# Kernel optimization log

Measured on AMD Instinct MI355X. Metric: run time of the kernel, lower is better.

The kernel has to match this reference:

```python
import jax, jax.numpy as jnp
import numpy as np
from jax import lax

VOCAB = 32000
EMBED = 1024
HIDDEN = 1024
ML = 64          # config.MAX_LENGTH
L = 50           # input sentence length
HH = HIDDEN // 2 # per-direction encoder hidden


def _lstm_cell(x, h, c, Wih, Whh, bih, bhh):
    # torch LSTM gate order: i, f, g, o
    g = x @ Wih.T + h @ Whh.T + bih + bhh
    i, f, gg, o = jnp.split(g, 4)
    i = jax.nn.sigmoid(i)
    f = jax.nn.sigmoid(f)
    gg = jnp.tanh(gg)
    o = jax.nn.sigmoid(o)
    c = f * c + i * gg
    return o * jnp.tanh(c), c


def setup_inputs() -> dict:
    key = jax.random.key(0)
    ks = jax.random.split(key, 24)
    def n(k, shape, s=0.05):
        return jax.random.normal(k, shape, jnp.float32) * s
    return {
        "x_tokens": jax.random.randint(ks[0], (L,), 0, VOCAB, jnp.int32),
        "allowed_mask": jnp.ones((VOCAB + ML,), jnp.float32),
        "embedding": n(ks[1], (VOCAB, EMBED)),
        # encoder bi-LSTM (two cells, each hidden//2)
        "Wih_f": n(ks[2], (4 * HH, EMBED)), "Whh_f": n(ks[3], (4 * HH, HH)),
        "bih_f": n(ks[4], (4 * HH,)), "bhh_f": n(ks[5], (4 * HH,)),
        "Wih_b": n(ks[6], (4 * HH, EMBED)), "Whh_b": n(ks[7], (4 * HH, HH)),
        "bih_b": n(ks[8], (4 * HH,)), "bhh_b": n(ks[9], (4 * HH,)),
        # decoder LSTM: input = embed + 2*hidden
        "Wih_d": n(ks[10], (4 * HIDDEN, EMBED + 2 * HIDDEN)),
        "Whh_d": n(ks[11], (4 * HIDDEN, HIDDEN)),
        "bih_d": n(ks[12], (4 * HIDDEN,)), "bhh_d": n(ks[13], (4 * HIDDEN,)),
        # attention: Linear(2*hidden -> MAX_LENGTH)
        "attn_W": n(ks[14], (ML, 2 * HIDDEN)), "attn_b": n(ks[15], (ML,)),
        # generate layer: Linear(hidden -> vocab)
        "gen_W": n(ks[16], (VOCAB, HIDDEN)), "gen_b": n(ks[17], (VOCAB,)),
        # copy layer: Linear(hidden -> hidden)
        "copy_W": n(ks[18], (HIDDEN, HIDDEN)), "copy_b": n(ks[19], (HIDDEN,)),
    }


def _forward(allowed_mask, embedding, Wih_f, Whh_f, bih_f, bhh_f,
             Wih_b, Whh_b, bih_b, bhh_b, Wih_d, Whh_d, bih_d, bhh_d,
             attn_W, attn_b, gen_W, gen_b, copy_W, copy_b, x_tokens):
    xemb = embedding[x_tokens]  # (L, EMBED)

    # --- encoder: two LSTM cells both stepped forward-in-time (as in the
    # original, where the bidirectional LSTM is called one token at a time) ---
    def enc_step(carry, xe):
        hf, cf, hb, cb = carry
        hf, cf = _lstm_cell(xe, hf, cf, Wih_f, Whh_f, bih_f, bhh_f)
        hb, cb = _lstm_cell(xe, hb, cb, Wih_b, Whh_b, bih_b, bhh_b)
        return (hf, cf, hb, cb), jnp.concatenate([hf, hb])

    z = jnp.zeros((HH,), xemb.dtype)
    (hf, cf, hb, cb), enc = lax.scan(enc_step, (z, z, z, z), xemb)
    enc_outs = jnp.zeros((ML, HIDDEN), xemb.dtype).at[:L].set(enc)  # padded buffer
    h0 = jnp.concatenate([hf, hb])  # (HIDDEN,) decoder init
    c0 = jnp.concatenate([cf, cb])

    copy_enc = jnp.tanh(enc_outs @ copy_W.T + copy_b)  # (ML, HIDDEN), loop-invariant
    pos = jnp.arange(ML)
    sent_pad = jnp.full((ML,), -1, jnp.int32).at[:L].set(x_tokens)
    sos_emb = embedding[0]

    def dec_step(carry, t):
        h, c, prev_probs, prev_word, dec_in = carry
        first = t == 0
        # attentive read
        a = jnp.concatenate([dec_in, h])  # (2*HIDDEN,)
        attw = jax.nn.softmax(a @ attn_W.T + attn_b)
        attentive = attw @ enc_outs  # (HIDDEN,)
        # selective (copy) read from previous step's copy probs
        pc = prev_probs[VOCAB:]
        m = ((pos >= 1) & (pos < L - 1) & (sent_pad != prev_word)).astype(pc.dtype)
        pc = pc * m
        s = pc.sum()
        pc = jnp.where(s > 0, pc / jnp.where(s > 0, s, 1.0), pc)
        selective = pc @ enc_outs
        zero = jnp.zeros_like(attentive)
        attentive = jnp.where(first, zero, attentive)
        selective = jnp.where(first, zero, selective)
        # decoder LSTM step
        h, c = _lstm_cell(jnp.concatenate([dec_in, selective, attentive]),
                          h, c, Wih_d, Whh_d, bih_d, bhh_d)
        gen = h @ gen_W.T + gen_b        # (VOCAB,)
        copy = copy_enc @ h              # (ML,)
        probs = jax.nn.softmax(jnp.concatenate([gen, copy]))
        dist = probs * allowed_mask
        # deterministic action (argmax in place of Categorical.sample)
        aidx = jnp.argmax(dist)
        is_voc = aidx < VOCAB
        src = sent_pad[jnp.clip(aidx - VOCAB, 0, L - 1)]
        action = jnp.where(is_voc, aidx, src).astype(jnp.int32)
        prob = dist[aidx] + jnp.where(
            is_voc, jnp.zeros((), dist.dtype), dist[jnp.clip(action, 0, VOCAB - 1)])
        new = (h, c, lax.stop_gradient(probs), action, embedding[action])
        return new, (h, prob, action)

    carry0 = (h0, c0, jnp.zeros((VOCAB + ML,), h0.dtype),
              jnp.array(-1, jnp.int32), sos_emb)
    _, (hs, probs, actions) = lax.scan(dec_step, carry0, jnp.arange(ML))
    states = jnp.concatenate([h0[None], hs])  # (ML+1, HIDDEN)
    return states, probs, actions


def reference(x_tokens, allowed_mask, embedding, Wih_f, Whh_f, bih_f, bhh_f,
              Wih_b, Whh_b, bih_b, bhh_b, Wih_d, Whh_d, bih_d, bhh_d,
              attn_W, attn_b, gen_W, gen_b, copy_W, copy_b):
    return _forward(allowed_mask, embedding, Wih_f, Whh_f, bih_f, bhh_f,
                    Wih_b, Whh_b, bih_b, bhh_b, Wih_d, Whh_d, bih_d, bhh_d,
                    attn_W, attn_b, gen_W, gen_b, copy_W, copy_b, x_tokens)
```

## Files before the change

### kernel.cpp

```cpp
#include <hip/hip_runtime.h>
#include <math.h>

#define L 50
#define ML 64
#define VOCAB 32000
#define EMBED 1024
#define HID 1024
#define HH 512
#define TOT (VOCAB+ML)
#define NPART 501

#define WS_ENC_GATES 0
#define WS_C_ENC     8192
#define WS_ENC_OUTS  10240
#define WS_COPY_ENC  75776
#define WS_H_DEC     141312
#define WS_C_DEC     143360
#define WS_X_DEC     145408
#define WS_DGATES    148480
#define WS_LOGITS    152576
#define WS_PARTS     184640
#define WS_ATTW      186688
#define WS_PC        186752
#define WS_ACT       186816
#define WS_G         186880
#define WS_G_END     (186880+8192*64)
#define WS_PREG      711168
#define WS_PREG_END  (711168+50*4096)
#define WS_AH        915968
#define WS_P         916032
#define WS_P_END     (916032+32000*64)

__device__ __forceinline__ float wred_sum(float v){
  #pragma unroll
  for(int o=32;o;o>>=1) v += __shfl_xor(v,o,64);
  return v;
}
__device__ __forceinline__ float wred_max(float v){
  #pragma unroll
  for(int o=32;o;o>>=1) v = fmaxf(v,__shfl_xor(v,o,64));
  return v;
}
__device__ __forceinline__ float sigm(float x){ return 1.0f/(1.0f+__expf(-x)); }
__device__ __forceinline__ float d4(float4 a, float4 b){ return a.x*b.x + a.y*b.y + a.z*b.z + a.w*b.w; }

__global__ __launch_bounds__(256) void k_enc_pre2(
  const int* __restrict__ xt, const float* __restrict__ emb,
  const float* __restrict__ Wih_f, const float* __restrict__ bih_f, const float* __restrict__ bhh_f,
  const float* __restrict__ Wih_b, const float* __restrict__ bih_b, const float* __restrict__ bhh_b,
  float* __restrict__ ws)
{
  __shared__ int toks[L];
  const int tid=threadIdx.x, b=blockIdx.x, wave=tid>>6, lane=tid&63;
  float* pg = ws + WS_PREG;
  if(tid<L) toks[tid]=xt[tid];
  float4 wih[2][4]; float bias[2];
  #pragma unroll
  for(int rr=0;rr<2;rr++){
    int r=b*8+wave*2+rr; bool isF=(r<2048); int rl=isF?r:(r-2048);
    const float* wp=(isF?Wih_f:Wih_b)+(size_t)rl*EMBED;
    #pragma unroll
    for(int c4=0;c4<4;c4++) wih[rr][c4]=*(const float4*)(wp+c4*256+lane*4);
    bias[rr]= isF?(bih_f[rl]+bhh_f[rl]):(bih_b[rl]+bhh_b[rl]);
  }
  __syncthreads();
  const float* er0 = emb + (size_t)toks[0]*EMBED;
  float4 e0=*(const float4*)(er0      +lane*4);
  float4 e1=*(const float4*)(er0+256  +lane*4);
  float4 e2=*(const float4*)(er0+512  +lane*4);
  float4 e3=*(const float4*)(er0+768  +lane*4);
  for(int t=0;t<L;t++){
    int tn = (t+1<L)? t+1 : t;
    const float* en = emb + (size_t)toks[tn]*EMBED;
    float4 n0=*(const float4*)(en      +lane*4);
    float4 n1=*(const float4*)(en+256  +lane*4);
    float4 n2=*(const float4*)(en+512  +lane*4);
    float4 n3=*(const float4*)(en+768  +lane*4);
    #pragma unroll
    for(int rr=0;rr<2;rr++){
      int r=b*8+wave*2+rr;
      float acc = d4(wih[rr][0],e0)+d4(wih[rr][1],e1)+d4(wih[rr][2],e2)+d4(wih[rr][3],e3);
      acc=wred_sum(acc);
      if(lane==0) pg[(size_t)t*4096+r]=acc+bias[rr];
    }
    e0=n0; e1=n1; e2=n2; e3=n3;
  }
}

__global__ __launch_bounds__(256) void k_enc_rec(
  const float* __restrict__ Whh_f, const float* __restrict__ Whh_b,
  float* __restrict__ ws, int t)
{
  __shared__ __align__(16) float h_lds[1024];
  const int tid=threadIdx.x, b=blockIdx.x, wave=tid>>6, lane=tid&63;
  float* gates   = ws + WS_ENC_GATES;
  float* c_enc   = ws + WS_C_ENC;
  float* enc_outs= ws + WS_ENC_OUTS;
  const float* pg = ws + WS_PREG + (size_t)t*4096;
  if(t>0){
    const float* gp = gates + ((t-1)&1)*4096;
    const float* cp = c_enc + (t&1)*1024;
    float* cw = c_enc + ((t-1)&1)*1024;
    for(int u=tid;u<1024;u+=256){
      int base=(u<512)?0:2048, uu=(u<512)?u:(u-512);
      float ig=gp[base+uu], fg=gp[base+512+uu], gg=gp[base+1024+uu], og=gp[base+1536+uu];
      float cprev=(t==1)?0.0f:cp[u];
      float c=sigm(fg)*cprev+sigm(ig)*tanhf(gg);
      float h=sigm(og)*tanhf(c);
      h_lds[u]=h;
      if(b==0){ cw[u]=c; enc_outs[(size_t)(t-1)*1024+u]=h; }
    }
  }
  __syncthreads();
  float* gw = gates + (t&1)*4096;
  #pragma unroll
  for(int rr=0;rr<2;rr++){
    int r=b*8+wave*2+rr; bool isF=(r<2048); int rl=isF?r:(r-2048);
    if(t==0){
      if(lane==0) gw[r]=pg[r];
    } else {
      const float* hr=(isF?Whh_f:Whh_b)+(size_t)rl*HH;
      const float* hs=&h_lds[isF?0:512];
      float acc=0.0f;
      #pragma unroll
      for(int c2=0;c2<2;c2++){
        int m=c2*256+lane*4;
        acc += d4(*(const float4*)(hr+m), *(const float4*)(&hs[m]));
      }
      acc=wred_sum(acc);
      if(lane==0) gw[r]=pg[r]+acc;
    }
  }
}

__global__ __launch_bounds__(256) void k_enc_step(
  const int* __restrict__ xt, const float* __restrict__ emb,
  const float* __restrict__ Wih_f, const float* __restrict__ Whh_f,
  const float* __restrict__ bih_f, const float* __restrict__ bhh_f,
  const float* __restrict__ Wih_b, const float* __restrict__ Whh_b,
  const float* __restrict__ bih_b, const float* __restrict__ bhh_b,
  float* __restrict__ ws, int t)
{
  __shared__ __align__(16) float h_lds[1024];
  __shared__ __align__(16) float xe[1024];
  const int tid = threadIdx.x;
  float* gates   = ws + WS_ENC_GATES;
  float* c_enc   = ws + WS_C_ENC;
  float* enc_outs= ws + WS_ENC_OUTS;
  {
    const int tok = xt[t];
    const float* er = emb + (size_t)tok*EMBED;
    for(int j=tid;j<1024;j+=256) xe[j]=er[j];
  }
  if(t>0){
    const float* gp = gates + ((t-1)&1)*4096;
    const float* cp = c_enc + (t&1)*1024;
    float* cw = c_enc + ((t-1)&1)*1024;
    for(int u=tid;u<1024;u+=256){
      int base=(u<512)?0:2048, uu=(u<512)?u:(u-512);
      float ig=gp[base+uu], fg=gp[base+512+uu], gg=gp[base+1024+uu], og=gp[base+1536+uu];
      float cprev=(t==1)?0.0f:cp[u];
      float c=sigm(fg)*cprev+sigm(ig)*tanhf(gg);
      float h=sigm(og)*tanhf(c);
      h_lds[u]=h;
      if(blockIdx.x==0){ cw[u]=c; enc_outs[(size_t)(t-1)*1024+u]=h; }
    }
  }
  __syncthreads();
  float* gw = gates + (t&1)*4096;
  const int wave=tid>>6, lane=tid&63;
  for(int rr=0;rr<2;rr++){
    int r=blockIdx.x*8+wave*2+rr;
    bool isF=(r<2048); int rl=isF?r:(r-2048);
    const float* Wih=isF?Wih_f:Wih_b;
    const float* Whh=isF?Whh_f:Whh_b;
    float bias=isF?(bih_f[rl]+bhh_f[rl]):(bih_b[rl]+bhh_b[rl]);
    const float* wr=Wih+(size_t)rl*EMBED;
    float acc=0.0f;
    #pragma unroll
    for(int c4=0;c4<4;c4++){
      int m=c4*256+lane*4;
      acc += d4(*(const float4*)(wr+m), *(const float4*)(&xe[m]));
    }
    if(t>0){
      const float* hr=Whh+(size_t)rl*HH;
      const float* hs=&h_lds[isF?0:512];
      #pragma unroll
      for(int c2=0;c2<2;c2++){
        int m=c2*256+lane*4;
        acc += d4(*(const float4*)(hr+m), *(const float4*)(&hs[m]));
      }
    }
    acc=wred_sum(acc);
    if(lane==0) gw[r]=acc+bias;
  }
}

__global__ __launch_bounds__(256) void k_copy_final(
  const float* __restrict__ emb,
  const float* __restrict__ copy_W, const float* __restrict__ copy_b,
  float* __restrict__ ws, float* __restrict__ out)
{
  __shared__ __align__(16) float hf[1024];
  const int tid=threadIdx.x, b=blockIdx.x, wave=tid>>6, lane=tid&63;
  float* gates = ws + WS_ENC_GATES;
  float* c_enc = ws + WS_C_ENC;
  float* enc_outs = ws + WS_ENC_OUTS;
  float* cenc = ws + WS_COPY_ENC;
  float* h_dec = ws + WS_H_DEC;
  float* c_dec = ws + WS_C_DEC;
  float* x_dec = ws + WS_X_DEC;
  {
    const float* gp = gates + ((L-1)&1)*4096;
    const float* cp = c_enc + ((L-2)&1)*1024;
    for(int u=tid;u<1024;u+=256){
      int base=(u<512)?0:2048, uu=(u<512)?u:(u-512);
      float ig=gp[base+uu], fg=gp[base+512+uu], gg=gp[base+1024+uu], og=gp[base+1536+uu];
      float c=sigm(fg)*cp[u]+sigm(ig)*tanhf(gg);
      float h=sigm(og)*tanhf(c);
      hf[u]=h;
      if(b==0){
        enc_outs[(size_t)(L-1)*1024+u]=h;
        h_dec[1024+u]=h;
        c_dec[1024+u]=c;
        out[u]=h;
      }
    }
    if(b==1) for(int j=tid;j<(ML-L)*1024;j+=256) enc_outs[(size_t)L*1024+j]=0.0f;
    if(b==2) for(int j=tid;j<1024;j+=256){
      x_dec[j]=emb[j];
      x_dec[1024+j]=0.0f;
      x_dec[2048+j]=0.0f;
    }
  }
  __syncthreads();
  int j = b*4 + wave;
  const float* wr = copy_W + (size_t)j*1024;
  float4 w0=*(const float4*)(wr+0*256+lane*4);
  float4 w1=*(const float4*)(wr+1*256+lane*4);
  float4 w2=*(const float4*)(wr+2*256+lane*4);
  float4 w3=*(const float4*)(wr+3*256+lane*4);
  float bj = copy_b[j];
  for(int k=0;k<L-1;k++){
    const float* er = enc_outs + (size_t)k*1024;
    float acc = d4(w0,*(const float4*)(er+0*256+lane*4))
              + d4(w1,*(const float4*)(er+1*256+lane*4))
              + d4(w2,*(const float4*)(er+2*256+lane*4))
              + d4(w3,*(const float4*)(er+3*256+lane*4));
    acc = wred_sum(acc);
    if(lane==0) cenc[(size_t)k*1024+j]=tanhf(acc+bj);
  }
  {
    float acc = d4(w0,*(const float4*)(&hf[0*256+lane*4]))
              + d4(w1,*(const float4*)(&hf[1*256+lane*4]))
              + d4(w2,*(const float4*)(&hf[2*256+lane*4]))
              + d4(w3,*(const float4*)(&hf[3*256+lane*4]));
    acc = wred_sum(acc);
    if(lane==0) cenc[(size_t)(L-1)*1024+j]=tanhf(acc+bj);
  }
  if(lane==0){
    float z=tanhf(0.0f+bj);
    for(int k=L;k<ML;k++) cenc[(size_t)k*1024+j]=z;
  }
}

__global__ __launch_bounds__(256) void k_gmat3(const float* __restrict__ Wih_d, float* __restrict__ ws)
{
  const int tid=threadIdx.x, wave=tid>>6, lane=tid&63;
  const float* enc = ws + WS_ENC_OUTS;
  float* G = ws + WS_G;
  float4 w[4][4];
  int rg[4];
  #pragma unroll
  for(int q=0;q<4;q++){
    int r = blockIdx.x*16 + wave*4 + q;
    rg[q]=r;
    const float* W = (r<4096) ? (Wih_d + (size_t)r*3072 + 1024)
                              : (Wih_d + (size_t)(r-4096)*3072 + 2048);
    #pragma unroll
    for(int c4=0;c4<4;c4++) w[q][c4]=*(const float4*)(W + c4*256 + lane*4);
  }
  const float* er0 = enc;
  float4 e0=*(const float4*)(er0      +lane*4);
  float4 e1=*(const float4*)(er0+256  +lane*4);
  float4 e2=*(const float4*)(er0+512  +lane*4);
  float4 e3=*(const float4*)(er0+768  +lane*4);
  for(int k=0;k<L;k++){
    int kn = (k+1<L)? k+1 : k;
    const float* en = enc + (size_t)kn*1024;
    float4 n0=*(const float4*)(en      +lane*4);
    float4 n1=*(const float4*)(en+256  +lane*4);
    float4 n2=*(const float4*)(en+512  +lane*4);
    float4 n3=*(const float4*)(en+768  +lane*4);
    #pragma unroll
    for(int q=0;q<4;q++){
      float acc = d4(w[q][0],e0)+d4(w[q][1],e1)+d4(w[q][2],e2)+d4(w[q][3],e3);
      acc=wred_sum(acc);
      if(lane==0) G[(size_t)rg[q]*64 + k]=acc;
    }
    e0=n0; e1=n1; e2=n2; e3=n3;
  }
  if(lane==0){
    #pragma unroll
    for(int q=0;q<4;q++)
      for(int kk=L;kk<64;kk++) G[(size_t)rg[q]*64 + kk]=0.0f;
  }
}

__global__ __launch_bounds__(256) void k_pmat5(
  const float* __restrict__ emb, const float* __restrict__ attn_W, float* __restrict__ ws)
{
  __shared__ float e_lds[64][68];
  __shared__ float w_lds[64][68];
  const int tid=threadIdx.x;
  const int wq=tid>>4, rq=tid&15;
  float* P = ws + WS_P;
  const int w0 = blockIdx.x*64;
  float acc[4][4];
  #pragma unroll
  for(int i=0;i<4;i++)
    #pragma unroll
    for(int j=0;j<4;j++) acc[i][j]=0.0f;
  for(int kc=0;kc<16;kc++){
    __syncthreads();
    #pragma unroll
    for(int v=0;v<4;v++){
      int idx=(v*256+tid)*4;
      int row=idx>>6, col=idx&63;
      float4 te=*(const float4*)(emb    + (size_t)(w0+row)*EMBED + kc*64 + col);
      *(float4*)&e_lds[row][col]=te;
      float4 tw=*(const float4*)(attn_W + (size_t)row*2048      + kc*64 + col);
      *(float4*)&w_lds[row][col]=tw;
    }
    __syncthreads();
    #pragma unroll
    for(int k4=0;k4<16;k4++){
      float4 e4[4], w4[4];
      #pragma unroll
      for(int i=0;i<4;i++) e4[i]=*(const float4*)&e_lds[wq+i*16][k4*4];
      #pragma unroll
      for(int j=0;j<4;j++) w4[j]=*(const float4*)&w_lds[rq+j*16][k4*4];
      #pragma unroll
      for(int i=0;i<4;i++)
        #pragma unroll
        for(int j=0;j<4;j++){
          acc[i][j] += e4[i].x*w4[j].x;
          acc[i][j] += e4[i].y*w4[j].y;
          acc[i][j] += e4[i].z*w4[j].z;
          acc[i][j] += e4[i].w*w4[j].w;
        }
    }
  }
  #pragma unroll
  for(int i=0;i<4;i++)
    #pragma unroll
    for(int j=0;j<4;j++)
      P[(size_t)(w0+wq+i*16)*64 + rq+j*16] = acc[i][j];
}

__global__ __launch_bounds__(256) void k_fin16(
  const int* __restrict__ xt, const float* __restrict__ amask,
  const float* __restrict__ emb,
  const float* __restrict__ attn_W, const float* __restrict__ attn_b,
  float* __restrict__ ws, float* __restrict__ out, int t, int fin_only)
{
  __shared__ __align__(16) float dec_in[1024];
  __shared__ __align__(16) float hprev[1024];
  __shared__ float r_lm[256], r_sm[256], r_ky[256];
  __shared__ int r_ix[256];
  __shared__ float s_lmax, s_Z;
  __shared__ int s_act;
  const int tid=threadIdx.x, b=blockIdx.x, wave=tid>>6, lane=tid&63;
  float* h_dec=ws+WS_H_DEC;
  float* logits=ws+WS_LOGITS; float* parts=ws+WS_PARTS;
  float* attw_raw=ws+WS_ATTW; float* pcw=ws+WS_PC;
  {
    float lm=-INFINITY, sm=0.0f, ky=-INFINITY; int ix=0x7fffffff;
    for(int i=tid;i<NPART;i+=256){
      const float4 p = *(const float4*)(parts+(size_t)i*4);
      float plm=p.x, psm=p.y, pky=p.z; int pix=__float_as_int(p.w);
      if(plm>lm){ sm = sm*__expf(lm-plm)+psm; lm=plm; }
      else sm += psm*__expf(plm-lm);
      if(pky>ky || (pky==ky && pix<ix)){ ky=pky; ix=pix; }
    }
    r_lm[tid]=lm; r_sm[tid]=sm; r_ky[tid]=ky; r_ix[tid]=ix;
    __syncthreads();
    for(int s=128;s;s>>=1){
      if(tid<s){
        float blm=r_lm[tid+s], bsm=r_sm[tid+s];
        float alm=r_lm[tid], a_sm=r_sm[tid];
        if(blm>alm){ r_sm[tid]=a_sm*__expf(alm-blm)+bsm; r_lm[tid]=blm; }
        else r_sm[tid]=a_sm+bsm*__expf(blm-alm);
        float bky=r_ky[tid+s]; int bix=r_ix[tid+s];
        if(bky>r_ky[tid] || (bky==r_ky[tid] && bix<r_ix[tid])){ r_ky[tid]=bky; r_ix[tid]=bix; }
      }
      __syncthreads();
    }
    if(tid==0){
      float lmax=r_lm[0]; float Z=r_sm[0];
      float bky=r_ky[0];
      int aidx = (bky==-INFINITY)?0:r_ix[0];
      bool isv = aidx<VOCAB;
      int kcl = aidx-VOCAB; kcl = kcl<0?0:(kcl>(L-1)?(L-1):kcl);
      int sp = xt[kcl];
      int action = isv? aidx : sp;
      if(b==0){
        float prob = amask[aidx]*__expf(logits[aidx]-lmax)/Z;
        if(!isv){
          int a2 = action<0?0:(action>(VOCAB-1)?(VOCAB-1):action);
          prob += amask[a2]*__expf(logits[a2]-lmax)/Z;
        }
        out[65*1024 + (t-1)] = prob;
        out[65*1024 + 64 + (t-1)] = (float)action;
        *(int*)(ws+WS_ACT) = action;
      }
      s_lmax=lmax; s_Z=Z; s_act=action;
    }
  }
  __syncthreads();
  if(fin_only) return;

  const int action = s_act;
  if(b==0 && tid<64){
    int k=tid;
    float v=__expf(logits[VOCAB+k]-s_lmax)/s_Z;
    int sp=(k<L)? xt[k] : -1;
    float m=(k>=1 && k<(L-1) && sp!=action)?1.0f:0.0f;
    float pv=v*m;
    float s=wred_sum(pv);
    pcw[k]=(s>0.0f)? pv/s : pv;
  }
  {
    int row = action<0 ? action+VOCAB : action;
    const float* er = emb + (size_t)row*EMBED;
    const float* hp = h_dec + ((t-1)&1)*1024;
    for(int j=tid;j<1024;j+=256){ dec_in[j]=er[j]; hprev[j]=hp[j]; }
  }
  __syncthreads();
  {
    int r = b*4 + wave;
    const float* wr = attn_W + (size_t)r*2048;
    float acc=0.0f;
    #pragma unroll
    for(int c4=0;c4<4;c4++){
      int m=c4*256+lane*4;
      acc += d4(*(const float4*)(wr+m),      *(const float4*)(&dec_in[m]));
      acc += d4(*(const float4*)(wr+1024+m), *(const float4*)(&hprev[m]));
    }
    acc=wred_sum(acc);
    if(lane==0) attw_raw[r]=acc+attn_b[r];
  }
}

__global__ __launch_bounds__(256) void k_dec_gates4(
  const int* __restrict__ xt, const float* __restrict__ amask,
  const float* __restrict__ emb, const float* __restrict__ attn_b,
  const float* __restrict__ Wih_d, const float* __restrict__ Whh_d,
  const float* __restrict__ bih_d, const float* __restrict__ bhh_d,
  float* __restrict__ ws, float* __restrict__ out, int t)
{
  __shared__ __align__(16) float di[1024];
  __shared__ __align__(16) float hh[1024];
  __shared__ float pcs[64], aws[64];
  __shared__ float r_lm[256], r_sm[256], r_ky[256];
  __shared__ int r_ix[256];
  __shared__ float s_lmax, s_Z;
  __shared__ int s_act;
  const int tid=threadIdx.x, b=blockIdx.x, wave=tid>>6, lane=tid&63;
  float* h_dec=ws+WS_H_DEC; float* dg=ws+WS_DGATES;
  float* logits=ws+WS_LOGITS; float* parts=ws+WS_PARTS;
  const float* G=ws+WS_G;

  if(t==0){
    for(int j=tid;j<1024;j+=256) di[j]=emb[j];
    if(tid<64){ pcs[tid]=0.0f; aws[tid]=0.0f; }
  } else {
    float lm=-INFINITY, sm=0.0f, ky=-INFINITY; int ix=0x7fffffff;
    for(int i=tid;i<NPART;i+=256){
      const float4 p = *(const float4*)(parts+(size_t)i*4);
      float plm=p.x, psm=p.y, pky=p.z; int pix=__float_as_int(p.w);
      if(plm>lm){ sm = sm*__expf(lm-plm)+psm; lm=plm; }
      else sm += psm*__expf(plm-lm);
      if(pky>ky || (pky==ky && pix<ix)){ ky=pky; ix=pix; }
    }
    r_lm[tid]=lm; r_sm[tid]=sm; r_ky[tid]=ky; r_ix[tid]=ix;
    __syncthreads();
    for(int s=128;s;s>>=1){
      if(tid<s){
        float blm=r_lm[tid+s], bsm=r_sm[tid+s];
        float alm=r_lm[tid], a_sm=r_sm[tid];
        if(blm>alm){ r_sm[tid]=a_sm*__expf(alm-blm)+bsm; r_lm[tid]=blm; }
        else r_sm[tid]=a_sm+bsm*__expf(blm-alm);
        float bky=r_ky[tid+s]; int bix=r_ix[tid+s];
        if(bky>r_ky[tid] || (bky==r_ky[tid] && bix<r_ix[tid])){ r_ky[tid]=bky; r_ix[tid]=bix; }
      }
      __syncthreads();
    }
    if(tid==0){
      float lmax=r_lm[0]; float Z=r_sm[0];
      float bky=r_ky[0];
      int aidx = (bky==-INFINITY)?0:r_ix[0];
      bool isv = aidx<VOCAB;
      int kcl = aidx-VOCAB; kcl = kcl<0?0:(kcl>(L-1)?(L-1):kcl);
      int sp = xt[kcl];
      int action = isv? aidx : sp;
      if(b==0){
        float prob = amask[aidx]*__expf(logits[aidx]-lmax)/Z;
        if(!isv){
          int a2 = action<0?0:(action>(VOCAB-1)?(VOCAB-1):action);
          prob += amask[a2]*__expf(logits[a2]-lmax)/Z;
        }
        out[65*1024 + (t-1)] = prob;
        out[65*1024 + 64 + (t-1)] = (float)action;
      }
      s_lmax=lmax; s_Z=Z; s_act=action;
    }
    __syncthreads();
    const int action = s_act;
    if(tid<64){
      int k=tid;
      float v=__expf(logits[VOCAB+k]-s_lmax)/s_Z;
      int sp=(k<L)? xt[k] : -1;
      float m=(k>=1 && k<(L-1) && sp!=action)?1.0f:0.0f;
      float pv=v*m;
      float s=wred_sum(pv);
      pcs[k]=(s>0.0f)? pv/s : pv;
    }
    __syncthreads();
    if(tid<64){
      float raw = (ws+WS_P)[(size_t)action*64 + tid] + (ws+WS_AH)[tid] + attn_b[tid];
      float mx=wred_max(raw);
      float e=__expf(raw-mx);
      float s=wred_sum(e);
      aws[tid]=e/s;
    }
    {
      const float* er = emb + (size_t)action*EMBED;
      for(int j=tid;j<1024;j+=256) di[j]=er[j];
    }
  }
  {
    const float* hp=h_dec+((t+1)&1)*1024;
    for(int j=tid;j<1024;j+=256) hh[j]=hp[j];
  }
  __syncthreads();
  for(int rr=0;rr<2;rr++){
    int r=b*8+wave*2+rr;
    const float* wd=Wih_d+(size_t)r*3072;
    float acc=0.0f;
    #pragma unroll
    for(int c4=0;c4<4;c4++){
      int m=c4*256+lane*4;
      acc += d4(*(const float4*)(wd+m), *(const float4*)(&di[m]));
    }
    const float* hr=Whh_d+(size_t)r*1024;
    #pragma unroll
    for(int c4=0;c4<4;c4++){
      int m=c4*256+lane*4;
      acc += d4(*(const float4*)(hr+m), *(const float4*)(&hh[m]));
    }
    acc += G[(size_t)r*64+lane]*pcs[lane];
    acc += G[(size_t)(4096+r)*64+lane]*aws[lane];
    acc=wred_sum(acc);
    if(lane==0) dg[r]=acc+bih_d[r]+bhh_d[r];
  }
}

__global__ __launch_bounds__(256) void k_dec_gates3(
  const float* __restrict__ emb,
  const float* __restrict__ Wih_d, const float* __restrict__ Whh_d,
  const float* __restrict__ bih_d, const float* __restrict__ bhh_d,
  float* __restrict__ ws, int t)
{
  __shared__ __align__(16) float di[1024];
  __shared__ __align__(16) float hh[1024];
  __shared__ float pcs[64], aws[64];
  const int tid=threadIdx.x;
  float* h_dec=ws+WS_H_DEC; float* dg=ws+WS_DGATES;
  const float* G=ws+WS_G;
  if(t==0){
    for(int j=tid;j<1024;j+=256) di[j]=emb[j];
    if(tid<64){ pcs[tid]=0.0f; aws[tid]=0.0f; }
  } else {
    const int action = *(const int*)(ws+WS_ACT);
    const float* er = emb + (size_t)action*EMBED;
    for(int j=tid;j<1024;j+=256) di[j]=er[j];
    if(tid<64){
      pcs[tid]=(ws+WS_PC)[tid];
      float v=(ws+WS_ATTW)[tid];
      float mx=wred_max(v);
      float e=__expf(v-mx);
      float s=wred_sum(e);
      aws[tid]=e/s;
    }
  }
  {
    const float* hp=h_dec+((t+1)&1)*1024;
    for(int j=tid;j<1024;j+=256) hh[j]=hp[j];
  }
  __syncthreads();
  const int wave=tid>>6, lane=tid&63;
  for(int rr=0;rr<2;rr++){
    int r=blockIdx.x*8+wave*2+rr;
    const float* wd=Wih_d+(size_t)r*3072;
    float acc=0.0f;
    #pragma unroll
    for(int c4=0;c4<4;c4++){
      int m=c4*256+lane*4;
      acc += d4(*(const float4*)(wd+m), *(const float4*)(&di[m]));
    }
    const float* hr=Whh_d+(size_t)r*1024;
    #pragma unroll
    for(int c4=0;c4<4;c4++){
      int m=c4*256+lane*4;
      acc += d4(*(const float4*)(hr+m), *(const float4*)(&hh[m]));
    }
    acc += G[(size_t)r*64+lane]*pcs[lane];
    acc += G[(size_t)(4096+r)*64+lane]*aws[lane];
    acc=wred_sum(acc);
    if(lane==0) dg[r]=acc+bih_d[r]+bhh_d[r];
  }
}

__global__ __launch_bounds__(256) void k_dec_gen2(
  const float* __restrict__ gen_W, const float* __restrict__ gen_b,
  const float* __restrict__ amask, const float* __restrict__ attn_W,
  float* __restrict__ ws, float* __restrict__ out, int t)
{
  __shared__ __align__(16) float h_lds[1024];
  __shared__ float w_lm[4], w_sm[4], w_ky[4];
  __shared__ int w_ix[4];
  const int tid=threadIdx.x;
  float* dg=ws+WS_DGATES;
  float* c_dec=ws+WS_C_DEC; float* h_dec=ws+WS_H_DEC;
  float* logits=ws+WS_LOGITS; float* parts=ws+WS_PARTS;
  float* cenc=ws+WS_COPY_ENC;
  {
    const float* cp=c_dec+((t+1)&1)*1024;
    float* cw=c_dec+(t&1)*1024;
    float* hw=h_dec+(t&1)*1024;
    for(int u=tid;u<1024;u+=256){
      float ig=dg[u], fg=dg[1024+u], gg=dg[2048+u], og=dg[3072+u];
      float c=sigm(fg)*cp[u]+sigm(ig)*tanhf(gg);
      float h=sigm(og)*tanhf(c);
      h_lds[u]=h;
      if(blockIdx.x==0){ cw[u]=c; hw[u]=h; out[(size_t)(t+1)*1024+u]=h; }
    }
  }
  __syncthreads();
  const int wave=tid>>6, lane=tid&63;
  const int b=blockIdx.x;
  if(b==501){
    float* AH=ws+WS_AH;
    for(int rr=0;rr<16;rr++){
      int r=wave*16+rr;
      const float* wr = attn_W + (size_t)r*2048 + 1024;
      float acc=0.0f;
      #pragma unroll
      for(int c4=0;c4<4;c4++){
        int m=c4*256+lane*4;
        acc += d4(*(const float4*)(wr+m), *(const float4*)(&h_lds[m]));
      }
      acc=wred_sum(acc);
      if(lane==0) AH[r]=acc;
    }
    return;
  }
  const bool isGen=(b<500);
  const int rbase = isGen ? (b*64+wave*16) : (VOCAB+wave*16);
  float lv[16];
  #pragma unroll
  for(int rr=0;rr<16;rr++){
    const float* wr = isGen ? gen_W+(size_t)(rbase+rr)*1024
                            : cenc +(size_t)(rbase-VOCAB+rr)*1024;
    float acc=0.0f;
    #pragma unroll
    for(int c4=0;c4<4;c4++){
      int m=c4*256+lane*4;
      acc += d4(*(const float4*)(wr+m), *(const float4*)(&h_lds[m]));
    }
    acc=wred_sum(acc);
    lv[rr] = isGen ? acc+gen_b[rbase+rr] : acc;
  }
  if(lane==0){
    float lm=-INFINITY, ky=-INFINITY; int ix=0;
    #pragma unroll
    for(int rr=0;rr<16;rr++){
      int gi=rbase+rr;
      logits[gi]=lv[rr];
      lm=fmaxf(lm,lv[rr]);
      float mk=amask[gi];
      float kk = (mk>0.0f)? (lv[rr]+__logf(mk)) : -INFINITY;
      if(kk>ky){ ky=kk; ix=gi; }
    }
    float sm=0.0f;
    #pragma unroll
    for(int rr=0;rr<16;rr++) sm += __expf(lv[rr]-lm);
    w_lm[wave]=lm; w_sm[wave]=sm; w_ky[wave]=ky; w_ix[wave]=ix;
  }
  __syncthreads();
  if(tid==0){
    float lm=w_lm[0], sm=w_sm[0], ky=w_ky[0]; int ix=w_ix[0];
    for(int w=1;w<4;w++){
      float blm=w_lm[w], bsm=w_sm[w];
      if(blm>lm){ sm=sm*__expf(lm-blm)+bsm; lm=blm; }
      else sm += bsm*__expf(blm-lm);
      if(w_ky[w]>ky || (w_ky[w]==ky && w_ix[w]<ix)){ ky=w_ky[w]; ix=w_ix[w]; }
    }
    float4 p; p.x=lm; p.y=sm; p.z=ky; p.w=__int_as_float(ix);
    *(float4*)(parts+(size_t)b*4)=p;
  }
}

extern "C" void kernel_launch(void* const* d_in, const int* in_sizes, int n_in,
                              void* d_out, int out_size, void* d_ws, size_t ws_size,
                              hipStream_t stream)
{
  const int*   xt     = (const int*)d_in[0];
  const float* amask  = (const float*)d_in[1];
  const float* emb    = (const float*)d_in[2];
  const float* Wih_f  = (const float*)d_in[3];
  const float* Whh_f  = (const float*)d_in[4];
  const float* bih_f  = (const float*)d_in[5];
  const float* bhh_f  = (const float*)d_in[6];
  const float* Wih_b  = (const float*)d_in[7];
  const float* Whh_b  = (const float*)d_in[8];
  const float* bih_b  = (const float*)d_in[9];
  const float* bhh_b  = (const float*)d_in[10];
  const float* Wih_d  = (const float*)d_in[11];
  const float* Whh_d  = (const float*)d_in[12];
  const float* bih_d  = (const float*)d_in[13];
  const float* bhh_d  = (const float*)d_in[14];
  const float* attn_W = (const float*)d_in[15];
  const float* attn_b = (const float*)d_in[16];
  const float* gen_W  = (const float*)d_in[17];
  const float* gen_b  = (const float*)d_in[18];
  const float* copy_W = (const float*)d_in[19];
  const float* copy_b = (const float*)d_in[20];
  float* out=(float*)d_out;
  float* ws =(float*)d_ws;

  const bool hasPreg = ws_size >= (size_t)WS_PREG_END*sizeof(float);
  const bool hasP    = ws_size >= (size_t)WS_P_END*sizeof(float);

  if(hasPreg){
    k_enc_pre2<<<512,256,0,stream>>>(xt,emb,Wih_f,bih_f,bhh_f,Wih_b,bih_b,bhh_b,ws);
    for(int t=0;t<L;t++)
      k_enc_rec<<<512,256,0,stream>>>(Whh_f,Whh_b,ws,t);
  } else {
    for(int t=0;t<L;t++)
      k_enc_step<<<512,256,0,stream>>>(xt,emb,Wih_f,Whh_f,bih_f,bhh_f,Wih_b,Whh_b,bih_b,bhh_b,ws,t);
  }
  k_copy_final<<<256,256,0,stream>>>(emb,copy_W,copy_b,ws,out);
  k_gmat3<<<512,256,0,stream>>>(Wih_d,ws);

  if(hasP){
    k_pmat5<<<500,256,0,stream>>>(emb,attn_W,ws);
    for(int t=0;t<ML;t++){
      k_dec_gates4<<<512,256,0,stream>>>(xt,amask,emb,attn_b,Wih_d,Whh_d,bih_d,bhh_d,ws,out,t);
      k_dec_gen2  <<<502,256,0,stream>>>(gen_W,gen_b,amask,attn_W,ws,out,t);
    }
    k_fin16<<<1,256,0,stream>>>(xt,amask,emb,attn_W,attn_b,ws,out,ML,1);
  } else {
    k_dec_gates3<<<512,256,0,stream>>>(emb,Wih_d,Whh_d,bih_d,bhh_d,ws,0);
    k_dec_gen2  <<<501,256,0,stream>>>(gen_W,gen_b,amask,attn_W,ws,out,0);
    for(int t=1;t<ML;t++){
      k_fin16     <<<16,256,0,stream>>>(xt,amask,emb,attn_W,attn_b,ws,out,t,0);
      k_dec_gates3<<<512,256,0,stream>>>(emb,Wih_d,Whh_d,bih_d,bhh_d,ws,t);
      k_dec_gen2  <<<501,256,0,stream>>>(gen_W,gen_b,amask,attn_W,ws,out,t);
    }
    k_fin16<<<1,256,0,stream>>>(xt,amask,emb,attn_W,attn_b,ws,out,ML,1);
  }
}
```

Baseline: 3.084 ms.

## Move argmax/softmax reduction into last-block of generate kernel via atomic ticket

The cross-block reduction of logit partials (softmax normaliser, argmax action, copy and attention weights) moves out of every one of the 512 gate blocks and into a single last-arriving block of the generate kernel. That block is chosen with an atomic counter per timestep. Gate blocks now just read the precomputed action, pc and attention weights from the workspace, which removes redundant reduction work and shortens the gate kernel's serial prologue. It adds a memset of the tickets, threadfences and a per-step tail run by one block, and it needs a larger workspace for the ticket array.

Measured after the change: 4.135 ms. +34.1%, slower.

```diff
diff --git a/kernel.cpp b/kernel.cpp
--- a/kernel.cpp
+++ b/kernel.cpp
@@ -30,6 +30,8 @@
 #define WS_AH        915968
 #define WS_P         916032
 #define WS_P_END     (916032+32000*64)
+#define WS_TICK      2964032
+#define WS_END3      (2964032+64)
 
 __device__ __forceinline__ float wred_sum(float v){
   #pragma unroll
@@ -452,92 +454,26 @@
   }
 }
 
-__global__ __launch_bounds__(256) void k_dec_gates4(
-  const int* __restrict__ xt, const float* __restrict__ amask,
-  const float* __restrict__ emb, const float* __restrict__ attn_b,
+__global__ __launch_bounds__(256) void k_dec_gates5(
+  const float* __restrict__ emb,
   const float* __restrict__ Wih_d, const float* __restrict__ Whh_d,
   const float* __restrict__ bih_d, const float* __restrict__ bhh_d,
-  float* __restrict__ ws, float* __restrict__ out, int t)
+  float* __restrict__ ws, int t)
 {
   __shared__ __align__(16) float di[1024];
   __shared__ __align__(16) float hh[1024];
   __shared__ float pcs[64], aws[64];
-  __shared__ float r_lm[256], r_sm[256], r_ky[256];
-  __shared__ int r_ix[256];
-  __shared__ float s_lmax, s_Z;
-  __shared__ int s_act;
   const int tid=threadIdx.x, b=blockIdx.x, wave=tid>>6, lane=tid&63;
   float* h_dec=ws+WS_H_DEC; float* dg=ws+WS_DGATES;
-  float* logits=ws+WS_LOGITS; float* parts=ws+WS_PARTS;
   const float* G=ws+WS_G;
-
   if(t==0){
     for(int j=tid;j<1024;j+=256) di[j]=emb[j];
     if(tid<64){ pcs[tid]=0.0f; aws[tid]=0.0f; }
   } else {
-    float lm=-INFINITY, sm=0.0f, ky=-INFINITY; int ix=0x7fffffff;
-    for(int i=tid;i<NPART;i+=256){
-      const float4 p = *(const float4*)(parts+(size_t)i*4);
-      float plm=p.x, psm=p.y, pky=p.z; int pix=__float_as_int(p.w);
-      if(plm>lm){ sm = sm*__expf(lm-plm)+psm; lm=plm; }
-      else sm += psm*__expf(plm-lm);
-      if(pky>ky || (pky==ky && pix<ix)){ ky=pky; ix=pix; }
-    }
-    r_lm[tid]=lm; r_sm[tid]=sm; r_ky[tid]=ky; r_ix[tid]=ix;
-    __syncthreads();
-    for(int s=128;s;s>>=1){
-      if(tid<s){
-        float blm=r_lm[tid+s], bsm=r_sm[tid+s];
-        float alm=r_lm[tid], a_sm=r_sm[tid];
-        if(blm>alm){ r_sm[tid]=a_sm*__expf(alm-blm)+bsm; r_lm[tid]=blm; }
-        else r_sm[tid]=a_sm+bsm*__expf(blm-alm);
-        float bky=r_ky[tid+s]; int bix=r_ix[tid+s];
-        if(bky>r_ky[tid] || (bky==r_ky[tid] && bix<r_ix[tid])){ r_ky[tid]=bky; r_ix[tid]=bix; }
-      }
-      __syncthreads();
-    }
-    if(tid==0){
-      float lmax=r_lm[0]; float Z=r_sm[0];
-      float bky=r_ky[0];
-      int aidx = (bky==-INFINITY)?0:r_ix[0];
-      bool isv = aidx<VOCAB;
-      int kcl = aidx-VOCAB; kcl = kcl<0?0:(kcl>(L-1)?(L-1):kcl);
-      int sp = xt[kcl];
-      int action = isv? aidx : sp;
-      if(b==0){
-        float prob = amask[aidx]*__expf(logits[aidx]-lmax)/Z;
-        if(!isv){
-          int a2 = action<0?0:(action>(VOCAB-1)?(VOCAB-1):action);
-          prob += amask[a2]*__expf(logits[a2]-lmax)/Z;
-        }
-        out[65*1024 + (t-1)] = prob;
-        out[65*1024 + 64 + (t-1)] = (float)action;
-      }
-      s_lmax=lmax; s_Z=Z; s_act=action;
-    }
-    __syncthreads();
-    const int action = s_act;
-    if(tid<64){
-      int k=tid;
-      float v=__expf(logits[VOCAB+k]-s_lmax)/s_Z;
-      int sp=(k<L)? xt[k] : -1;
-      float m=(k>=1 && k<(L-1) && sp!=action)?1.0f:0.0f;
-      float pv=v*m;
-      float s=wred_sum(pv);
-      pcs[k]=(s>0.0f)? pv/s : pv;
-    }
-    __syncthreads();
-    if(tid<64){
-      float raw = (ws+WS_P)[(size_t)action*64 + tid] + (ws+WS_AH)[tid] + attn_b[tid];
-      float mx=wred_max(raw);
-      float e=__expf(raw-mx);
-      float s=wred_sum(e);
-      aws[tid]=e/s;
-    }
-    {
-      const float* er = emb + (size_t)action*EMBED;
-      for(int j=tid;j<1024;j+=256) di[j]=er[j];
-    }
+    const int action = *(const int*)(ws+WS_ACT);
+    const float* er = emb + (size_t)action*EMBED;
+    for(int j=tid;j<1024;j+=256) di[j]=er[j];
+    if(tid<64){ pcs[tid]=(ws+WS_PC)[tid]; aws[tid]=(ws+WS_ATTW)[tid]; }
   }
   {
     const float* hp=h_dec+((t+1)&1)*1024;
@@ -619,6 +555,168 @@
     acc += G[(size_t)(4096+r)*64+lane]*aws[lane];
     acc=wred_sum(acc);
     if(lane==0) dg[r]=acc+bih_d[r]+bhh_d[r];
+  }
+}
+
+__global__ __launch_bounds__(256) void k_dec_gen3(
+  const int* __restrict__ xt, const float* __restrict__ amask,
+  const float* __restrict__ gen_W, const float* __restrict__ gen_b,
+  const float* __restrict__ attn_W, const float* __restrict__ attn_b,
+  float* __restrict__ ws, float* __restrict__ out, int t)
+{
+  __shared__ __align__(16) float h_lds[1024];
+  __shared__ float w_lm[4], w_sm[4], w_ky[4];
+  __shared__ int w_ix[4];
+  __shared__ float r_lm[256], r_sm[256], r_ky[256];
+  __shared__ int r_ix[256];
+  __shared__ float s_lmax, s_Z;
+  __shared__ int s_act, s_old;
+  const int tid=threadIdx.x, b=blockIdx.x, wave=tid>>6, lane=tid&63;
+  float* dg=ws+WS_DGATES;
+  float* c_dec=ws+WS_C_DEC; float* h_dec=ws+WS_H_DEC;
+  float* logits=ws+WS_LOGITS; float* parts=ws+WS_PARTS;
+  float* cenc=ws+WS_COPY_ENC;
+  {
+    const float* cp=c_dec+((t+1)&1)*1024;
+    float* cw=c_dec+(t&1)*1024;
+    float* hw=h_dec+(t&1)*1024;
+    for(int u=tid;u<1024;u+=256){
+      float ig=dg[u], fg=dg[1024+u], gg=dg[2048+u], og=dg[3072+u];
+      float c=sigm(fg)*cp[u]+sigm(ig)*tanhf(gg);
+      float h=sigm(og)*tanhf(c);
+      h_lds[u]=h;
+      if(b==0){ cw[u]=c; hw[u]=h; out[(size_t)(t+1)*1024+u]=h; }
+    }
+  }
+  __syncthreads();
+  if(b==501){
+    float* AH=ws+WS_AH;
+    for(int rr=0;rr<16;rr++){
+      int r=wave*16+rr;
+      const float* wr = attn_W + (size_t)r*2048 + 1024;
+      float acc=0.0f;
+      #pragma unroll
+      for(int c4=0;c4<4;c4++){
+        int m=c4*256+lane*4;
+        acc += d4(*(const float4*)(wr+m), *(const float4*)(&h_lds[m]));
+      }
+      acc=wred_sum(acc);
+      if(lane==0) AH[r]=acc;
+    }
+  } else {
+    const bool isGen=(b<500);
+    const int rbase = isGen ? (b*64+wave*16) : (VOCAB+wave*16);
+    float lv[16];
+    #pragma unroll
+    for(int rr=0;rr<16;rr++){
+      const float* wr = isGen ? gen_W+(size_t)(rbase+rr)*1024
+                              : cenc +(size_t)(rbase-VOCAB+rr)*1024;
+      float acc=0.0f;
+      #pragma unroll
+      for(int c4=0;c4<4;c4++){
+        int m=c4*256+lane*4;
+        acc += d4(*(const float4*)(wr+m), *(const float4*)(&h_lds[m]));
+      }
+      acc=wred_sum(acc);
+      lv[rr] = isGen ? acc+gen_b[rbase+rr] : acc;
+    }
+    if(lane==0){
+      float lm=-INFINITY, ky=-INFINITY; int ix=0;
+      #pragma unroll
+      for(int rr=0;rr<16;rr++){
+        int gi=rbase+rr;
+        logits[gi]=lv[rr];
+        lm=fmaxf(lm,lv[rr]);
+        float mk=amask[gi];
+        float kk = (mk>0.0f)? (lv[rr]+__logf(mk)) : -INFINITY;
+        if(kk>ky){ ky=kk; ix=gi; }
+      }
+      float sm=0.0f;
+      #pragma unroll
+      for(int rr=0;rr<16;rr++) sm += __expf(lv[rr]-lm);
+      w_lm[wave]=lm; w_sm[wave]=sm; w_ky[wave]=ky; w_ix[wave]=ix;
+    }
+    __syncthreads();
+    if(tid==0){
+      float lm=w_lm[0], sm=w_sm[0], ky=w_ky[0]; int ix=w_ix[0];
+      for(int w=1;w<4;w++){
+        float blm=w_lm[w], bsm=w_sm[w];
+        if(blm>lm){ sm=sm*__expf(lm-blm)+bsm; lm=blm; }
+        else sm += bsm*__expf(blm-lm);
+        if(w_ky[w]>ky || (w_ky[w]==ky && w_ix[w]<ix)){ ky=w_ky[w]; ix=w_ix[w]; }
+      }
+      float4 p; p.x=lm; p.y=sm; p.z=ky; p.w=__int_as_float(ix);
+      *(float4*)(parts+(size_t)b*4)=p;
+    }
+  }
+
+  __syncthreads();
+  if(tid==0){
+    __threadfence();
+    s_old=__hip_atomic_fetch_add((int*)(ws+WS_TICK)+t,1,__ATOMIC_ACQ_REL,__HIP_MEMORY_SCOPE_AGENT);
+  }
+  __syncthreads();
+  if(s_old!=(int)gridDim.x-1) return;
+  if(tid==0) __threadfence();
+  __syncthreads();
+
+  {
+    float lm=-INFINITY, sm=0.0f, ky=-INFINITY; int ix=0x7fffffff;
+    for(int i=tid;i<NPART;i+=256){
+      const float4 p = *(const float4*)(parts+(size_t)i*4);
+      float plm=p.x, psm=p.y, pky=p.z; int pix=__float_as_int(p.w);
+      if(plm>lm){ sm = sm*__expf(lm-plm)+psm; lm=plm; }
+      else sm += psm*__expf(plm-lm);
+      if(pky>ky || (pky==ky && pix<ix)){ ky=pky; ix=pix; }
+    }
+    r_lm[tid]=lm; r_sm[tid]=sm; r_ky[tid]=ky; r_ix[tid]=ix;
+    __syncthreads();
+    for(int s=128;s;s>>=1){
+      if(tid<s){
+        float blm=r_lm[tid+s], bsm=r_sm[tid+s];
+        float alm=r_lm[tid], a_sm=r_sm[tid];
+        if(blm>alm){ r_sm[tid]=a_sm*__expf(alm-blm)+bsm; r_lm[tid]=blm; }
+        else r_sm[tid]=a_sm+bsm*__expf(blm-alm);
+        float bky=r_ky[tid+s]; int bix=r_ix[tid+s];
+        if(bky>r_ky[tid] || (bky==r_ky[tid] && bix<r_ix[tid])){ r_ky[tid]=bky; r_ix[tid]=bix; }
+      }
+      __syncthreads();
+    }
+    if(tid==0){
+      float lmax=r_lm[0]; float Z=r_sm[0];
+      float bky=r_ky[0];
+      int aidx = (bky==-INFINITY)?0:r_ix[0];
+      bool isv = aidx<VOCAB;
+      int kcl = aidx-VOCAB; kcl = kcl<0?0:(kcl>(L-1)?(L-1):kcl);
+      int sp = xt[kcl];
+      int action = isv? aidx : sp;
+      float prob = amask[aidx]*__expf(logits[aidx]-lmax)/Z;
+      if(!isv){
+        int a2 = action<0?0:(action>(VOCAB-1)?(VOCAB-1):action);
+        prob += amask[a2]*__expf(logits[a2]-lmax)/Z;
+      }
+      out[65*1024 + t]      = prob;
+      out[65*1024 + 64 + t] = (float)action;
+      *(int*)(ws+WS_ACT) = action;
+      s_lmax=lmax; s_Z=Z; s_act=action;
+    }
+  }
+  __syncthreads();
+  if(t==ML-1) return;
+  const int action=s_act;
+  if(tid<64){
+    int k=tid;
+    float v=__expf(logits[VOCAB+k]-s_lmax)/s_Z;
+    int sp=(k<L)? xt[k] : -1;
+    float m=(k>=1 && k<(L-1) && sp!=action)?1.0f:0.0f;
+    float pv=v*m;
+    float s=wred_sum(pv);
+    (ws+WS_PC)[k]=(s>0.0f)? pv/s : pv;
+    float raw = (ws+WS_P)[(size_t)action*64 + k] + (ws+WS_AH)[k] + attn_b[k];
+    float mx=wred_max(raw);
+    float e=__expf(raw-mx);
+    float s2=wred_sum(e);
+    (ws+WS_ATTW)[k]=e/s2;
   }
 }
 
@@ -741,7 +839,7 @@
   float* ws =(float*)d_ws;
 
   const bool hasPreg = ws_size >= (size_t)WS_PREG_END*sizeof(float);
-  const bool hasP    = ws_size >= (size_t)WS_P_END*sizeof(float);
+  const bool hasP    = ws_size >= (size_t)WS_END3*sizeof(float);
 
   if(hasPreg){
     k_enc_pre2<<<512,256,0,stream>>>(xt,emb,Wih_f,bih_f,bhh_f,Wih_b,bih_b,bhh_b,ws);
@@ -755,12 +853,12 @@
   k_gmat3<<<512,256,0,stream>>>(Wih_d,ws);
 
   if(hasP){
+    hipMemsetAsync((char*)d_ws + (size_t)WS_TICK*sizeof(float), 0, 64*sizeof(int), stream);
     k_pmat5<<<500,256,0,stream>>>(emb,attn_W,ws);
     for(int t=0;t<ML;t++){
-      k_dec_gates4<<<512,256,0,stream>>>(xt,amask,emb,attn_b,Wih_d,Whh_d,bih_d,bhh_d,ws,out,t);
-      k_dec_gen2  <<<502,256,0,stream>>>(gen_W,gen_b,amask,attn_W,ws,out,t);
-    }
-    k_fin16<<<1,256,0,stream>>>(xt,amask,emb,attn_W,attn_b,ws,out,ML,1);
+      k_dec_gates5<<<512,256,0,stream>>>(emb,Wih_d,Whh_d,bih_d,bhh_d,ws,t);
+      k_dec_gen3  <<<502,256,0,stream>>>(xt,amask,gen_W,gen_b,attn_W,attn_b,ws,out,t);
+    }
   } else {
     k_dec_gates3<<<512,256,0,stream>>>(emb,Wih_d,Whh_d,bih_d,bhh_d,ws,0);
     k_dec_gen2  <<<501,256,0,stream>>>(gen_W,gen_b,amask,attn_W,ws,out,0);
```
